# Kernel tuning notes

Measured on AMD Instinct MI355X. Metric: run time of the kernel, lower is better.

## Reference

```python
import jax, jax.numpy as jnp
import numpy as np

NUM_HEADS = 8  # init num_heads


def setup_inputs() -> dict:
    key = jax.random.key(0)
    ks = jax.random.split(key, 8)
    B, N, C, G = 2, 256 * 256, 256, 512  # N hardcoded by original reshape(256*256)
    xq = jax.random.normal(ks[0], (B, N, C), jnp.float32)
    xk = jax.random.normal(ks[1], (B, N, C), jnp.float32)
    xv = jax.random.normal(ks[2], (B, N, C), jnp.float32)
    w_scale = C ** -0.5
    Wq = jax.random.normal(ks[3], (C, C), jnp.float32) * w_scale
    bq = jax.random.normal(ks[4], (C,), jnp.float32) * 0.02
    Wp = jax.random.normal(ks[5], (C, C), jnp.float32) * w_scale
    bp = jax.random.normal(ks[6], (C,), jnp.float32) * 0.02
    # Voronoi cell labels 1..G, each cell exactly N//G tokens, randomly scattered
    # over the 256x256 grid (irregular gather/scatter access, all cells < 1500 tokens).
    labels = jnp.repeat(jnp.arange(1, G + 1, dtype=jnp.int32), N // G)
    Voronoi = jnp.stack([
        jax.random.permutation(jax.random.fold_in(ks[7], b), labels) for b in range(B)
    ]).reshape(B, 256, 256)
    return {"xq": xq, "xk": xk, "xv": xv, "Wq": Wq, "bq": bq,
            "Wp": Wp, "bp": bp, "Voronoi": Voronoi, "num_groups": G}


def reference(xq, xk, xv, Wq, bq, Wp, bp, Voronoi, num_groups):
    B, N, C = xq.shape
    H = NUM_HEADS
    hd = C // H
    scale = hd ** -0.5  # qk_scale default: head_dim ** -0.5
    # NOTE: the original forward projects q, k AND v with self.q (shared weights/bias).
    # This (likely a bug upstream) is preserved faithfully here.
    q = (xq @ Wq.T + bq).reshape(B, N, H, hd)
    k = (xk @ Wq.T + bq).reshape(B, N, H, hd)
    v = (xv @ Wq.T + bq).reshape(B, N, H, hd)
    labels = Voronoi.reshape(B, N)
    order = jnp.argsort(labels, axis=1)   # [B, N] sort tokens by Voronoi cell id
    inv = jnp.argsort(order, axis=1)      # inverse permutation for scatter-back
    S = N // num_groups                   # tokens per cell (static)

    def gather(t):  # [B, N, H, hd] -> [B, G, S, H, hd] grouped by cell
        return jnp.take_along_axis(t, order[:, :, None, None], axis=1).reshape(B, num_groups, S, H, hd)

    qg = gather(q) * scale
    kg = gather(k)
    vg = gather(v)
    attn = jnp.einsum('bgshd,bgthd->bghst', qg, kg)   # per-cell scores [B,G,H,S,S]
    p = jax.nn.softmax(attn, axis=-1)                 # attn_drop=0 (eval)
    og = jnp.einsum('bghst,bgthd->bgshd', p, vg).reshape(B, N, H, hd)
    out = jnp.take_along_axis(og, inv[:, :, None, None], axis=1).reshape(B, N, C)
    return out @ Wp.T + bp                            # proj_drop=0 (eval)
```

## Files before the change

### kernel.cpp

```cpp
#include <hip/hip_runtime.h>
#include <hip/hip_bf16.h>

#define B_    2
#define NTOK  65536
#define C_    256
#define H_    8
#define HD_   32
#define G_    512
#define S_    128
#define BN    (B_*NTOK)
#define M3    (3*BN)

typedef __attribute__((ext_vector_type(8))) short short8;
typedef __attribute__((ext_vector_type(4))) float f32x4;

__device__ __forceinline__ ushort f2bf(float f) {
  __bf16 h = (__bf16)f;
  return __builtin_bit_cast(unsigned short, h);
}
__device__ __forceinline__ unsigned pk2(float lo, float hi) {
  return (unsigned)f2bf(lo) | ((unsigned)f2bf(hi) << 16);
}

__device__ __forceinline__ void gl16(const void* g, void* l) {
  __builtin_amdgcn_global_load_lds(
      (const __attribute__((address_space(1))) unsigned int*)g,
      (__attribute__((address_space(3))) unsigned int*)l, 16, 0, 0);
}

#define SW4(c, r) ((((c) ^ (r) ^ ((r) >> 2))) & 3)
#define SWK32(c, r) ((((c) ^ ((r) >> 1))) & 3)
#define VSL(c, ch) ((((c) ^ (((ch) & 7) << 1) ^ (((ch) >> 3) & 3))) & 15)

#define QSCALE 0.25506907131737264f

__global__ __launch_bounds__(256) void k_prep(const float* __restrict__ Wq,
                                              const float* __restrict__ Wp,
                                              ushort* __restrict__ Wq_img,
                                              ushort* __restrict__ Wp_img) {
  int gid = blockIdx.x * 256 + threadIdx.x;
  int w = gid >> 13, rem = gid & 8191;
  if (w == 0) {
    int ks = rem >> 11, rem2 = rem & 2047;
    int r = rem2 >> 3, c = rem2 & 7;
    const float4* s = reinterpret_cast<const float4*>(Wq + (size_t)r * 256 + ks * 64 + c * 8);
    float4 a = s[0], b = s[1];
    uint4 o;
    o.x = pk2(a.x, a.y); o.y = pk2(a.z, a.w);
    o.z = pk2(b.x, b.y); o.w = pk2(b.z, b.w);
    *reinterpret_cast<uint4*>(Wq_img + ks * 16384 + r * 64 + ((c ^ (r & 7)) << 3)) = o;
  } else {
    int h = rem >> 10, r = (rem >> 2) & 255, c = rem & 3;
    const float4* s = reinterpret_cast<const float4*>(Wp + (size_t)r * 256 + h * 32 + c * 8);
    float4 a = s[0], b = s[1];
    uint4 o;
    o.x = pk2(a.x, a.y); o.y = pk2(a.z, a.w);
    o.z = pk2(b.x, b.y); o.w = pk2(b.z, b.w);
    *reinterpret_cast<uint4*>(Wp_img + h * 8192 + r * 32 + (SWK32(c, r) << 3)) = o;
  }
}

__global__ __launch_bounds__(256) void k_group(const int* __restrict__ vor,
                                               int* __restrict__ grp,
                                               int* __restrict__ cnt) {
  int idx = blockIdx.x * 256 + threadIdx.x;
  int b = idx >> 16;
  int n = idx & (NTOK - 1);
  int g = vor[idx] - 1;
  int pos = atomicAdd(&cnt[(b << 9) + g], 1);
  grp[((b << 9) + g) * S_ + pos] = n;
}

__global__ __launch_bounds__(512, 4) void k_proj_qkv(
    const float* __restrict__ xq, const float* __restrict__ xk,
    const float* __restrict__ xv, const ushort* __restrict__ Wq_img,
    const float* __restrict__ bq, ushort* __restrict__ qkv) {
  __shared__ ushort As[128 * 64];
  __shared__ ushort Bs[2][256 * 64];
  int mt = blockIdx.x;
  int t = mt >> 10;
  const float* A = (t == 0) ? xq : (t == 1) ? xk : xv;
  float qsc = (t == 0) ? QSCALE : 1.0f;
  size_t abase = (size_t)(mt & 1023) * 128 * 256;
  int row0 = mt * 128;

  int tid = threadIdx.x, lane = tid & 63, wave = tid >> 6;
  int l15 = lane & 15, hi = lane >> 4;
  int wr = (wave >> 2) * 64, wc = (wave & 3) * 64;
  int sr = tid >> 2, sq = tid & 3;

  const float* aptr = A + abase + (size_t)sr * 256 + sq * 16;
  int boff = wave * 4096 + lane * 16;

  f32x4 acc[4][4] = {};
  float4 ar[2][4];
  {
    const float4* p = reinterpret_cast<const float4*>(aptr);
#pragma unroll
    for (int j = 0; j < 4; ++j) ar[0][j] = p[j];
  }
#pragma unroll
  for (int j = 0; j < 4; ++j)
    gl16((const char*)Wq_img + boff + j * 1024, (char*)Bs[0] + boff + j * 1024);

#pragma unroll
  for (int ks = 0; ks < 4; ++ks) {
    uint4 w0, w1;
    w0.x = pk2(ar[ks & 1][0].x, ar[ks & 1][0].y); w0.y = pk2(ar[ks & 1][0].z, ar[ks & 1][0].w);
    w0.z = pk2(ar[ks & 1][1].x, ar[ks & 1][1].y); w0.w = pk2(ar[ks & 1][1].z, ar[ks & 1][1].w);
    w1.x = pk2(ar[ks & 1][2].x, ar[ks & 1][2].y); w1.y = pk2(ar[ks & 1][2].z, ar[ks & 1][2].w);
    w1.z = pk2(ar[ks & 1][3].x, ar[ks & 1][3].y); w1.w = pk2(ar[ks & 1][3].z, ar[ks & 1][3].w);
    *reinterpret_cast<uint4*>(&As[sr * 64 + (((sq * 2) ^ (sr & 7)) << 3)]) = w0;
    *reinterpret_cast<uint4*>(&As[sr * 64 + (((sq * 2 + 1) ^ (sr & 7)) << 3)]) = w1;
    if (ks < 3) {
      const float4* p = reinterpret_cast<const float4*>(aptr + (ks + 1) * 64);
#pragma unroll
      for (int j = 0; j < 4; ++j) ar[(ks + 1) & 1][j] = p[j];
#pragma unroll
      for (int j = 0; j < 4; ++j)
        gl16((const char*)Wq_img + (ks + 1) * 32768 + boff + j * 1024,
             (char*)Bs[(ks + 1) & 1] + boff + j * 1024);
      asm volatile("s_waitcnt vmcnt(8)" ::: "memory");
    } else {
      asm volatile("s_waitcnt vmcnt(0)" ::: "memory");
    }
    asm volatile("s_waitcnt lgkmcnt(0)" ::: "memory");
    __builtin_amdgcn_s_barrier();
    const ushort* Bcur = Bs[ks & 1];
#pragma unroll
    for (int kk = 0; kk < 2; ++kk) {
      int ck = kk * 4 + hi;
      short8 af[4], bfr[4];
#pragma unroll
      for (int m = 0; m < 4; ++m) {
        int r = wr + m * 16 + l15;
        af[m] = *reinterpret_cast<const short8*>(&As[r * 64 + ((ck ^ (r & 7)) << 3)]);
      }
#pragma unroll
      for (int n = 0; n < 4; ++n) {
        int r = wc + n * 16 + l15;
        bfr[n] = *reinterpret_cast<const short8*>(&Bcur[r * 64 + ((ck ^ (r & 7)) << 3)]);
      }
#pragma unroll
      for (int m = 0; m < 4; ++m)
#pragma unroll
        for (int n = 0; n < 4; ++n)
          acc[m][n] = __builtin_amdgcn_mfma_f32_16x16x32_bf16(af[m], bfr[n], acc[m][n], 0, 0, 0);
    }
    asm volatile("s_waitcnt lgkmcnt(0)" ::: "memory");
    __builtin_amdgcn_s_barrier();
  }

  ushort* Ot = (ushort*)Bs;
#pragma unroll
  for (int n = 0; n < 4; ++n) {
    int col = wc + n * 16 + l15;
    float bv = bq[col];
    int c = col >> 3, ci = col & 7;
#pragma unroll
    for (int m = 0; m < 4; ++m) {
      int r0 = wr + m * 16 + hi * 4;
#pragma unroll
      for (int j = 0; j < 4; ++j) {
        int r = r0 + j;
        int slot = c ^ (((r >> 2) & 3) << 1);
        Ot[r * 256 + slot * 8 + ci] = f2bf((acc[m][n][j] + bv) * qsc);
      }
    }
  }
  __syncthreads();
  {
    size_t gbase = (size_t)row0 * 256;
#pragma unroll
    for (int s = 0; s < 8; ++s) {
      int off = s * 4096 + tid * 8;
      int r = off >> 8, cc = (off >> 3) & 31;
      int slot = cc ^ (((r >> 2) & 3) << 1);
      *reinterpret_cast<uint4*>(qkv + gbase + off) =
          *reinterpret_cast<const uint4*>(Ot + r * 256 + slot * 8);
    }
  }
}

__global__ __launch_bounds__(512) void k_attn_proj(
    const ushort* __restrict__ qkv, const int* __restrict__ grp,
    const ushort* __restrict__ Wp_img, const float* __restrict__ bp,
    float* __restrict__ out) {
  __shared__ int toks[128];
  __shared__ ushort shm[32768];
  ushort* Qs  = shm;
  ushort* Ks  = shm + 4096;
  ushort* Vt  = shm + 8192;
  ushort* Oh  = shm + 12288;
  ushort* Wp0 = shm + 16384;
  ushort* Wp1 = shm + 24576;

  int bid = blockIdx.x;
  int g = bid & (G_ - 1), b = bid >> 9;
  int tid = threadIdx.x, lane = tid & 63, wave = tid >> 6;
  int l15 = lane & 15, hi = lane >> 4;
  int strip = wave * 16;
  int mg = wave >> 1, ng = wave & 1;

  if (tid < 128) toks[tid] = grp[((b << 9) + g) * S_ + tid];
  __syncthreads();

  int wpoff = wave * 1024 + lane * 16;
  gl16((const char*)Wp_img + wpoff, (char*)Wp0 + wpoff);
  gl16((const char*)Wp_img + 8192 + wpoff, (char*)Wp0 + wpoff + 8192);

  f32x4 acc[2][8] = {};

  int r_st = tid >> 2, cp = tid & 3;
  int tok_st = toks[r_st];
  size_t rowq = (size_t)(b * NTOK + tok_st) * 256;
  int chunk_t = r_st >> 3, tl = r_st & 7;

  uint4 qa, ka, va;
  {
    size_t base = rowq + cp * 8;
    qa = *reinterpret_cast<const uint4*>(qkv + base);
    ka = *reinterpret_cast<const uint4*>(qkv + (size_t)BN * 256 + base);
    va = *reinterpret_cast<const uint4*>(qkv + (size_t)2 * BN * 256 + base);
  }

  for (int h = 0; h < 8; ++h) {
    ushort* WpCur = (h & 1) ? Wp1 : Wp0;
    ushort* WpNext = (h & 1) ? Wp0 : Wp1;
    *reinterpret_cast<uint4*>(&Qs[r_st * 32 + SW4(cp, r_st) * 8]) = qa;
    *reinterpret_cast<uint4*>(&Ks[r_st * 32 + SW4(cp, r_st) * 8]) = ka;
    {
      const ushort* pv_ = reinterpret_cast<const ushort*>(&va);
#pragma unroll
      for (int e = 0; e < 8; ++e) {
        int ch = cp * 8 + e;
        Vt[ch * 128 + (VSL(chunk_t, ch) << 3) + tl] = pv_[e];
      }
    }
    asm volatile("s_waitcnt lgkmcnt(0)" ::: "memory");
    __builtin_amdgcn_s_barrier();

    if (h < 7) {
      gl16((const char*)Wp_img + (h + 1) * 16384 + wpoff, (char*)WpNext + wpoff);
      gl16((const char*)Wp_img + (h + 1) * 16384 + 8192 + wpoff, (char*)WpNext + wpoff + 8192);
      size_t base = rowq + (h + 1) * 32 + cp * 8;
      qa = *reinterpret_cast<const uint4*>(qkv + base);
      ka = *reinterpret_cast<const uint4*>(qkv + (size_t)BN * 256 + base);
      va = *reinterpret_cast<const uint4*>(qkv + (size_t)2 * BN * 256 + base);
    }

    f32x4 sacc[8] = {};
    {
      int ra = strip + l15;
      short8 qf = *reinterpret_cast<const short8*>(&Qs[ra * 32 + SW4(hi, ra) * 8]);
#pragma unroll
      for (int n = 0; n < 8; ++n) {
        int r = n * 16 + l15;
        short8 kf = *reinterpret_cast<const short8*>(&Ks[r * 32 + SW4(hi, r) * 8]);
        sacc[n] = __builtin_amdgcn_mfma_f32_16x16x32_bf16(kf, qf, sacc[n], 0, 0, 0);
      }
    }

    float mx = -1e30f;
#pragma unroll
    for (int n = 0; n < 8; ++n)
#pragma unroll
      for (int j = 0; j < 4; ++j) mx = fmaxf(mx, sacc[n][j]);
    mx = fmaxf(mx, __shfl_xor(mx, 16));
    mx = fmaxf(mx, __shfl_xor(mx, 32));
    float p[8][4];
    float sum = 0.f;
#pragma unroll
    for (int n = 0; n < 8; ++n)
#pragma unroll
      for (int j = 0; j < 4; ++j) { p[n][j] = exp2f(sacc[n][j] - mx); sum += p[n][j]; }
    sum += __shfl_xor(sum, 16);
    sum += __shfl_xor(sum, 32);
    float inv = 1.0f / sum;

    short8 paf[4];
#pragma unroll
    for (int t = 0; t < 4; ++t) {
      unsigned e0 = pk2(p[2 * t][0], p[2 * t][1]);
      unsigned e1 = pk2(p[2 * t][2], p[2 * t][3]);
      unsigned o0 = pk2(p[2 * t + 1][0], p[2 * t + 1][1]);
      unsigned o1 = pk2(p[2 * t + 1][2], p[2 * t + 1][3]);
      unsigned pe0 = __shfl_xor(e0, 16), pe1 = __shfl_xor(e1, 16);
      unsigned po0 = __shfl_xor(o0, 16), po1 = __shfl_xor(o1, 16);
      bool up = (hi & 1);
      unsigned E0 = up ? pe0 : e0, E1 = up ? pe1 : e1;
      unsigned E2 = up ? e0 : pe0, E3 = up ? e1 : pe1;
      unsigned O0 = up ? po0 : o0, O1 = up ? po1 : o1;
      unsigned O2 = up ? o0 : po0, O3 = up ? o1 : po1;
      unsigned s0 = up ? E0 : O0, s1 = up ? E1 : O1;
      unsigned s2 = up ? E2 : O2, s3 = up ? E3 : O3;
      unsigned r0 = __shfl_xor(s0, 32), r1 = __shfl_xor(s1, 32);
      unsigned r2 = __shfl_xor(s2, 32), r3 = __shfl_xor(s3, 32);
      unsigned f0, f1, f2, f3;
      if (hi == 0)      { f0 = E0; f1 = E1; f2 = E2; f3 = E3; }
      else if (hi == 3) { f0 = O0; f1 = O1; f2 = O2; f3 = O3; }
      else              { f0 = r0; f1 = r1; f2 = r2; f3 = r3; }
      union { unsigned u[4]; short8 s; } cv;
      cv.u[0] = f0; cv.u[1] = f1; cv.u[2] = f2; cv.u[3] = f3;
      paf[t] = cv.s;
    }

    f32x4 oacc[2] = {};
#pragma unroll
    for (int t = 0; t < 4; ++t) {
      short8 bv[2];
#pragma unroll
      for (int n2 = 0; n2 < 2; ++n2) {
        int ch = n2 * 16 + l15;
        int chunk = t * 4 + hi;
        bv[n2] = *reinterpret_cast<const short8*>(&Vt[ch * 128 + (VSL(chunk, ch) << 3)]);
      }
#pragma unroll
      for (int n2 = 0; n2 < 2; ++n2)
        oacc[n2] = __builtin_amdgcn_mfma_f32_16x16x32_bf16(paf[t], bv[n2], oacc[n2], 0, 0, 0);
    }

    float invj[4];
#pragma unroll
    for (int jr = 0; jr < 4; ++jr) invj[jr] = __shfl(inv, hi * 4 + jr);
#pragma unroll
    for (int n2 = 0; n2 < 2; ++n2)
#pragma unroll
      for (int jr = 0; jr < 4; ++jr) {
        int row = strip + hi * 4 + jr;
        int col = n2 * 16 + l15;
        Oh[row * 32 + (SWK32(col >> 3, row) << 3) + (col & 7)] = f2bf(oacc[n2][jr] * invj[jr]);
      }
    asm volatile("s_waitcnt vmcnt(5)" ::: "memory");
    asm volatile("s_waitcnt lgkmcnt(0)" ::: "memory");
    __builtin_amdgcn_s_barrier();

    {
      short8 af[2], bf[8];
#pragma unroll
      for (int m = 0; m < 2; ++m) {
        int r = mg * 32 + m * 16 + l15;
        af[m] = *reinterpret_cast<const short8*>(&Oh[r * 32 + (SWK32(hi, r) << 3)]);
      }
#pragma unroll
      for (int n = 0; n < 8; ++n) {
        int r = ng * 128 + n * 16 + l15;
        bf[n] = *reinterpret_cast<const short8*>(&WpCur[r * 32 + (SWK32(hi, r) << 3)]);
      }
#pragma unroll
      for (int m = 0; m < 2; ++m)
#pragma unroll
        for (int n = 0; n < 8; ++n)
          acc[m][n] = __builtin_amdgcn_mfma_f32_16x16x32_bf16(af[m], bf[n], acc[m][n], 0, 0, 0);
    }
  }

  float* Of = (float*)shm;
#pragma unroll
  for (int q = 0; q < 4; ++q) {
    __syncthreads();
    if (mg == q) {
#pragma unroll
      for (int n = 0; n < 8; ++n) {
        int col = ng * 128 + n * 16 + l15;
        float bv = bp[col];
        int c = col >> 2, ci = col & 3;
#pragma unroll
        for (int m = 0; m < 2; ++m) {
#pragma unroll
          for (int j = 0; j < 4; ++j) {
            int lr = m * 16 + hi * 4 + j;
            int slot = c ^ (((lr >> 2) & 3) << 2);
            Of[lr * 256 + slot * 4 + ci] = acc[m][n][j] + bv;
          }
        }
      }
    }
    __syncthreads();
#pragma unroll
    for (int s = 0; s < 4; ++s) {
      int off = s * 2048 + tid * 4;
      int lr = off >> 8, cc = (off >> 2) & 63;
      int slot = cc ^ (((lr >> 2) & 3) << 2);
      int tok = toks[q * 32 + lr];
      *reinterpret_cast<float4*>(out + ((size_t)(b * NTOK + tok)) * 256 + cc * 4) =
          *reinterpret_cast<const float4*>(Of + lr * 256 + slot * 4);
    }
  }
}

extern "C" void kernel_launch(void* const* d_in, const int* in_sizes, int n_in,
                              void* d_out, int out_size, void* d_ws, size_t ws_size,
                              hipStream_t stream) {
  const float* xq = (const float*)d_in[0];
  const float* xk = (const float*)d_in[1];
  const float* xv = (const float*)d_in[2];
  const float* Wq = (const float*)d_in[3];
  const float* bq = (const float*)d_in[4];
  const float* Wp = (const float*)d_in[5];
  const float* bp = (const float*)d_in[6];
  const int*   vor = (const int*)d_in[7];

  char* ws = (char*)d_ws;
  ushort* qkv    = (ushort*)ws;
  int*    grp    = (int*)(ws + (size_t)201326592);
  int*    cnt    = (int*)(ws + (size_t)201850880);
  ushort* Wq_img = (ushort*)(ws + (size_t)201854976);
  ushort* Wp_img = (ushort*)(ws + (size_t)201986048);

  hipMemsetAsync(cnt, 0, B_ * G_ * sizeof(int), stream);
  k_prep<<<dim3(64), dim3(256), 0, stream>>>(Wq, Wp, Wq_img, Wp_img);
  k_group<<<dim3(BN / 256), dim3(256), 0, stream>>>(vor, grp, cnt);
  k_proj_qkv<<<dim3(M3 / 128), dim3(512), 0, stream>>>(xq, xk, xv, Wq_img, bq, qkv);
  k_attn_proj<<<dim3(B_ * G_), dim3(512), 0, stream>>>(qkv, grp, Wp_img, bp, (float*)d_out);
}
```

Measured before the change: 316.0 us.

## Stage V for all heads upfront, process head pairs, load Wp into registers

The attention+projection kernel now loads the full V tile for all 8 heads into a large transposed LDS buffer before the loop. It stages Q/K two heads at a time with double buffers to halve the barriers per head. Wp fragments are read directly from global memory into registers (unswizzled image) instead of being staged through LDS with async copies. The trade-off is much larger LDS use, which reduces occupancy, plus extra register pressure and global-latency exposure for the Wp loads.

```diff
diff --git a/kernel.cpp b/kernel.cpp
--- a/kernel.cpp
+++ b/kernel.cpp
@@ -56,7 +56,7 @@
     uint4 o;
     o.x = pk2(a.x, a.y); o.y = pk2(a.z, a.w);
     o.z = pk2(b.x, b.y); o.w = pk2(b.z, b.w);
-    *reinterpret_cast<uint4*>(Wp_img + h * 8192 + r * 32 + (SWK32(c, r) << 3)) = o;
+    *reinterpret_cast<uint4*>(Wp_img + h * 8192 + r * 32 + c * 8) = o;
   }
 }
 
@@ -187,13 +187,14 @@
     const ushort* __restrict__ Wp_img, const float* __restrict__ bp,
     float* __restrict__ out) {
   __shared__ int toks[128];
-  __shared__ ushort shm[32768];
-  ushort* Qs  = shm;
-  ushort* Ks  = shm + 4096;
-  ushort* Vt  = shm + 8192;
-  ushort* Oh  = shm + 12288;
-  ushort* Wp0 = shm + 16384;
-  ushort* Wp1 = shm + 24576;
+  __shared__ ushort shm[57344];
+  ushort* Vt  = shm;
+  ushort* Qs0 = shm + 32768;
+  ushort* Qs1 = shm + 36864;
+  ushort* Ks0 = shm + 40960;
+  ushort* Ks1 = shm + 45056;
+  ushort* Oh0 = shm + 49152;
+  ushort* Oh1 = shm + 53248;
 
   int bid = blockIdx.x;
   int g = bid & (G_ - 1), b = bid >> 9;
@@ -205,10 +206,6 @@
   if (tid < 128) toks[tid] = grp[((b << 9) + g) * S_ + tid];
   __syncthreads();
 
-  int wpoff = wave * 1024 + lane * 16;
-  gl16((const char*)Wp_img + wpoff, (char*)Wp0 + wpoff);
-  gl16((const char*)Wp_img + 8192 + wpoff, (char*)Wp0 + wpoff + 8192);
-
   f32x4 acc[2][8] = {};
 
   int r_st = tid >> 2, cp = tid & 3;
@@ -216,142 +213,161 @@
   size_t rowq = (size_t)(b * NTOK + tok_st) * 256;
   int chunk_t = r_st >> 3, tl = r_st & 7;
 
-  uint4 qa, ka, va;
-  {
-    size_t base = rowq + cp * 8;
-    qa = *reinterpret_cast<const uint4*>(qkv + base);
-    ka = *reinterpret_cast<const uint4*>(qkv + (size_t)BN * 256 + base);
-    va = *reinterpret_cast<const uint4*>(qkv + (size_t)2 * BN * 256 + base);
-  }
-
+#pragma unroll
   for (int h = 0; h < 8; ++h) {
-    ushort* WpCur = (h & 1) ? Wp1 : Wp0;
-    ushort* WpNext = (h & 1) ? Wp0 : Wp1;
-    *reinterpret_cast<uint4*>(&Qs[r_st * 32 + SW4(cp, r_st) * 8]) = qa;
-    *reinterpret_cast<uint4*>(&Ks[r_st * 32 + SW4(cp, r_st) * 8]) = ka;
-    {
-      const ushort* pv_ = reinterpret_cast<const ushort*>(&va);
-#pragma unroll
-      for (int e = 0; e < 8; ++e) {
-        int ch = cp * 8 + e;
-        Vt[ch * 128 + (VSL(chunk_t, ch) << 3) + tl] = pv_[e];
-      }
-    }
+    uint4 v = *reinterpret_cast<const uint4*>(qkv + (size_t)2 * BN * 256 + rowq + h * 32 + cp * 8);
+    const ushort* pv_ = reinterpret_cast<const ushort*>(&v);
+#pragma unroll
+    for (int e = 0; e < 8; ++e) {
+      int ch = h * 32 + cp * 8 + e;
+      Vt[ch * 128 + (VSL(chunk_t, ch) << 3) + tl] = pv_[e];
+    }
+  }
+
+  uint4 qa2[2], ka2[2];
+#pragma unroll
+  for (int e = 0; e < 2; ++e) {
+    size_t base = rowq + e * 32 + cp * 8;
+    qa2[e] = *reinterpret_cast<const uint4*>(qkv + base);
+    ka2[e] = *reinterpret_cast<const uint4*>(qkv + (size_t)BN * 256 + base);
+  }
+  short8 bfreg[8];
+#pragma unroll
+  for (int n = 0; n < 8; ++n) {
+    int r = ng * 128 + n * 16 + l15;
+    bfreg[n] = *reinterpret_cast<const short8*>(Wp_img + r * 32 + hi * 8);
+  }
+
+#pragma unroll
+  for (int hp = 0; hp < 4; ++hp) {
+    *reinterpret_cast<uint4*>(&Qs0[r_st * 32 + SW4(cp, r_st) * 8]) = qa2[0];
+    *reinterpret_cast<uint4*>(&Ks0[r_st * 32 + SW4(cp, r_st) * 8]) = ka2[0];
+    *reinterpret_cast<uint4*>(&Qs1[r_st * 32 + SW4(cp, r_st) * 8]) = qa2[1];
+    *reinterpret_cast<uint4*>(&Ks1[r_st * 32 + SW4(cp, r_st) * 8]) = ka2[1];
     asm volatile("s_waitcnt lgkmcnt(0)" ::: "memory");
     __builtin_amdgcn_s_barrier();
 
-    if (h < 7) {
-      gl16((const char*)Wp_img + (h + 1) * 16384 + wpoff, (char*)WpNext + wpoff);
-      gl16((const char*)Wp_img + (h + 1) * 16384 + 8192 + wpoff, (char*)WpNext + wpoff + 8192);
-      size_t base = rowq + (h + 1) * 32 + cp * 8;
-      qa = *reinterpret_cast<const uint4*>(qkv + base);
-      ka = *reinterpret_cast<const uint4*>(qkv + (size_t)BN * 256 + base);
-      va = *reinterpret_cast<const uint4*>(qkv + (size_t)2 * BN * 256 + base);
-    }
-
-    f32x4 sacc[8] = {};
-    {
-      int ra = strip + l15;
-      short8 qf = *reinterpret_cast<const short8*>(&Qs[ra * 32 + SW4(hi, ra) * 8]);
-#pragma unroll
-      for (int n = 0; n < 8; ++n) {
-        int r = n * 16 + l15;
-        short8 kf = *reinterpret_cast<const short8*>(&Ks[r * 32 + SW4(hi, r) * 8]);
-        sacc[n] = __builtin_amdgcn_mfma_f32_16x16x32_bf16(kf, qf, sacc[n], 0, 0, 0);
-      }
-    }
-
-    float mx = -1e30f;
-#pragma unroll
-    for (int n = 0; n < 8; ++n)
-#pragma unroll
-      for (int j = 0; j < 4; ++j) mx = fmaxf(mx, sacc[n][j]);
-    mx = fmaxf(mx, __shfl_xor(mx, 16));
-    mx = fmaxf(mx, __shfl_xor(mx, 32));
-    float p[8][4];
-    float sum = 0.f;
-#pragma unroll
-    for (int n = 0; n < 8; ++n)
-#pragma unroll
-      for (int j = 0; j < 4; ++j) { p[n][j] = exp2f(sacc[n][j] - mx); sum += p[n][j]; }
-    sum += __shfl_xor(sum, 16);
-    sum += __shfl_xor(sum, 32);
-    float inv = 1.0f / sum;
-
-    short8 paf[4];
-#pragma unroll
-    for (int t = 0; t < 4; ++t) {
-      unsigned e0 = pk2(p[2 * t][0], p[2 * t][1]);
-      unsigned e1 = pk2(p[2 * t][2], p[2 * t][3]);
-      unsigned o0 = pk2(p[2 * t + 1][0], p[2 * t + 1][1]);
-      unsigned o1 = pk2(p[2 * t + 1][2], p[2 * t + 1][3]);
-      unsigned pe0 = __shfl_xor(e0, 16), pe1 = __shfl_xor(e1, 16);
-      unsigned po0 = __shfl_xor(o0, 16), po1 = __shfl_xor(o1, 16);
-      bool up = (hi & 1);
-      unsigned E0 = up ? pe0 : e0, E1 = up ? pe1 : e1;
-      unsigned E2 = up ? e0 : pe0, E3 = up ? e1 : pe1;
-      unsigned O0 = up ? po0 : o0, O1 = up ? po1 : o1;
-      unsigned O2 = up ? o0 : po0, O3 = up ? o1 : po1;
-      unsigned s0 = up ? E0 : O0, s1 = up ? E1 : O1;
-      unsigned s2 = up ? E2 : O2, s3 = up ? E3 : O3;
-      unsigned r0 = __shfl_xor(s0, 32), r1 = __shfl_xor(s1, 32);
-      unsigned r2 = __shfl_xor(s2, 32), r3 = __shfl_xor(s3, 32);
-      unsigned f0, f1, f2, f3;
-      if (hi == 0)      { f0 = E0; f1 = E1; f2 = E2; f3 = E3; }
-      else if (hi == 3) { f0 = O0; f1 = O1; f2 = O2; f3 = O3; }
-      else              { f0 = r0; f1 = r1; f2 = r2; f3 = r3; }
-      union { unsigned u[4]; short8 s; } cv;
-      cv.u[0] = f0; cv.u[1] = f1; cv.u[2] = f2; cv.u[3] = f3;
-      paf[t] = cv.s;
-    }
-
-    f32x4 oacc[2] = {};
-#pragma unroll
-    for (int t = 0; t < 4; ++t) {
-      short8 bv[2];
-#pragma unroll
-      for (int n2 = 0; n2 < 2; ++n2) {
-        int ch = n2 * 16 + l15;
-        int chunk = t * 4 + hi;
-        bv[n2] = *reinterpret_cast<const short8*>(&Vt[ch * 128 + (VSL(chunk, ch) << 3)]);
-      }
+    if (hp < 3) {
+#pragma unroll
+      for (int e = 0; e < 2; ++e) {
+        size_t base = rowq + (hp * 2 + 2 + e) * 32 + cp * 8;
+        qa2[e] = *reinterpret_cast<const uint4*>(qkv + base);
+        ka2[e] = *reinterpret_cast<const uint4*>(qkv + (size_t)BN * 256 + base);
+      }
+    }
+
+#pragma unroll
+    for (int e = 0; e < 2; ++e) {
+      const int h = hp * 2 + e;
+      const ushort* QsC = e ? Qs1 : Qs0;
+      const ushort* KsC = e ? Ks1 : Ks0;
+      ushort* OhC = e ? Oh1 : Oh0;
+
+      f32x4 sacc[8] = {};
+      {
+        int ra = strip + l15;
+        short8 qf = *reinterpret_cast<const short8*>(&QsC[ra * 32 + SW4(hi, ra) * 8]);
+#pragma unroll
+        for (int n = 0; n < 8; ++n) {
+          int r = n * 16 + l15;
+          short8 kf = *reinterpret_cast<const short8*>(&KsC[r * 32 + SW4(hi, r) * 8]);
+          sacc[n] = __builtin_amdgcn_mfma_f32_16x16x32_bf16(kf, qf, sacc[n], 0, 0, 0);
+        }
+      }
+
+      float mx = -1e30f;
+#pragma unroll
+      for (int n = 0; n < 8; ++n)
+#pragma unroll
+        for (int j = 0; j < 4; ++j) mx = fmaxf(mx, sacc[n][j]);
+      mx = fmaxf(mx, __shfl_xor(mx, 16));
+      mx = fmaxf(mx, __shfl_xor(mx, 32));
+      float p[8][4];
+      float sum = 0.f;
+#pragma unroll
+      for (int n = 0; n < 8; ++n)
+#pragma unroll
+        for (int j = 0; j < 4; ++j) { p[n][j] = exp2f(sacc[n][j] - mx); sum += p[n][j]; }
+      sum += __shfl_xor(sum, 16);
+      sum += __shfl_xor(sum, 32);
+      float inv = 1.0f / sum;
+
+      short8 paf[4];
+#pragma unroll
+      for (int t = 0; t < 4; ++t) {
+        unsigned e0 = pk2(p[2 * t][0], p[2 * t][1]);
+        unsigned e1 = pk2(p[2 * t][2], p[2 * t][3]);
+        unsigned o0 = pk2(p[2 * t + 1][0], p[2 * t + 1][1]);
+        unsigned o1 = pk2(p[2 * t + 1][2], p[2 * t + 1][3]);
+        unsigned pe0 = __shfl_xor(e0, 16), pe1 = __shfl_xor(e1, 16);
+        unsigned po0 = __shfl_xor(o0, 16), po1 = __shfl_xor(o1, 16);
+        bool up = (hi & 1);
+        unsigned E0 = up ? pe0 : e0, E1 = up ? pe1 : e1;
+        unsigned E2 = up ? e0 : pe0, E3 = up ? e1 : pe1;
+        unsigned O0 = up ? po0 : o0, O1 = up ? po1 : o1;
+        unsigned O2 = up ? o0 : po0, O3 = up ? o1 : po1;
+        unsigned s0 = up ? E0 : O0, s1 = up ? E1 : O1;
+        unsigned s2 = up ? E2 : O2, s3 = up ? E3 : O3;
+        unsigned r0 = __shfl_xor(s0, 32), r1 = __shfl_xor(s1, 32);
+        unsigned r2 = __shfl_xor(s2, 32), r3 = __shfl_xor(s3, 32);
+        unsigned f0, f1, f2, f3;
+        if (hi == 0)      { f0 = E0; f1 = E1; f2 = E2; f3 = E3; }
+        else if (hi == 3) { f0 = O0; f1 = O1; f2 = O2; f3 = O3; }
+        else              { f0 = r0; f1 = r1; f2 = r2; f3 = r3; }
+        union { unsigned u[4]; short8 s; } cv;
+        cv.u[0] = f0; cv.u[1] = f1; cv.u[2] = f2; cv.u[3] = f3;
+        paf[t] = cv.s;
+      }
+
+      f32x4 oacc[2] = {};
+#pragma unroll
+      for (int t = 0; t < 4; ++t) {
+        short8 bv[2];
+#pragma unroll
+        for (int n2 = 0; n2 < 2; ++n2) {
+          int ch = h * 32 + n2 * 16 + l15;
+          int chunk = t * 4 + hi;
+          bv[n2] = *reinterpret_cast<const short8*>(&Vt[ch * 128 + (VSL(chunk, ch) << 3)]);
+        }
+#pragma unroll
+        for (int n2 = 0; n2 < 2; ++n2)
+          oacc[n2] = __builtin_amdgcn_mfma_f32_16x16x32_bf16(paf[t], bv[n2], oacc[n2], 0, 0, 0);
+      }
+
+      float invj[4];
+#pragma unroll
+      for (int jr = 0; jr < 4; ++jr) invj[jr] = __shfl(inv, hi * 4 + jr);
 #pragma unroll
       for (int n2 = 0; n2 < 2; ++n2)
-        oacc[n2] = __builtin_amdgcn_mfma_f32_16x16x32_bf16(paf[t], bv[n2], oacc[n2], 0, 0, 0);
-    }
-
-    float invj[4];
-#pragma unroll
-    for (int jr = 0; jr < 4; ++jr) invj[jr] = __shfl(inv, hi * 4 + jr);
-#pragma unroll
-    for (int n2 = 0; n2 < 2; ++n2)
-#pragma unroll
-      for (int jr = 0; jr < 4; ++jr) {
-        int row = strip + hi * 4 + jr;
-        int col = n2 * 16 + l15;
-        Oh[row * 32 + (SWK32(col >> 3, row) << 3) + (col & 7)] = f2bf(oacc[n2][jr] * invj[jr]);
-      }
-    asm volatile("s_waitcnt vmcnt(5)" ::: "memory");
-    asm volatile("s_waitcnt lgkmcnt(0)" ::: "memory");
-    __builtin_amdgcn_s_barrier();
-
-    {
-      short8 af[2], bf[8];
-#pragma unroll
-      for (int m = 0; m < 2; ++m) {
-        int r = mg * 32 + m * 16 + l15;
-        af[m] = *reinterpret_cast<const short8*>(&Oh[r * 32 + (SWK32(hi, r) << 3)]);
-      }
-#pragma unroll
-      for (int n = 0; n < 8; ++n) {
-        int r = ng * 128 + n * 16 + l15;
-        bf[n] = *reinterpret_cast<const short8*>(&WpCur[r * 32 + (SWK32(hi, r) << 3)]);
-      }
-#pragma unroll
-      for (int m = 0; m < 2; ++m)
-#pragma unroll
-        for (int n = 0; n < 8; ++n)
-          acc[m][n] = __builtin_amdgcn_mfma_f32_16x16x32_bf16(af[m], bf[n], acc[m][n], 0, 0, 0);
+#pragma unroll
+        for (int jr = 0; jr < 4; ++jr) {
+          int row = strip + hi * 4 + jr;
+          int col = n2 * 16 + l15;
+          OhC[row * 32 + (SWK32(col >> 3, row) << 3) + (col & 7)] = f2bf(oacc[n2][jr] * invj[jr]);
+        }
+      asm volatile("s_waitcnt lgkmcnt(0)" ::: "memory");
+      __builtin_amdgcn_s_barrier();
+
+      {
+        short8 af[2];
+#pragma unroll
+        for (int m = 0; m < 2; ++m) {
+          int r = mg * 32 + m * 16 + l15;
+          af[m] = *reinterpret_cast<const short8*>(&OhC[r * 32 + (SWK32(hi, r) << 3)]);
+        }
+#pragma unroll
+        for (int m = 0; m < 2; ++m)
+#pragma unroll
+          for (int n = 0; n < 8; ++n)
+            acc[m][n] = __builtin_amdgcn_mfma_f32_16x16x32_bf16(af[m], bfreg[n], acc[m][n], 0, 0, 0);
+      }
+      if (h < 7) {
+#pragma unroll
+        for (int n = 0; n < 8; ++n) {
+          int r = ng * 128 + n * 16 + l15;
+          bfreg[n] = *reinterpret_cast<const short8*>(Wp_img + (h + 1) * 8192 + r * 32 + hi * 8);
+        }
+      }
     }
   }
 
```

Result: slower. 326.4 us (+3.3%).
